# Kernel optimization log

Hardware: AMD Instinct MI355X
Metric: run time of the kernel (lower is better)

Reference implementation:

```python
import jax, jax.numpy as jnp
import numpy as np

N = 50000
E = 1600000
F_IN = 128
F_OUT = 64
NEG_SLOPE = 0.2


def setup_inputs() -> dict:
    key = jax.random.key(0)
    k1, k2, k3, k4, k5, k6 = jax.random.split(key, 6)
    x = jax.random.normal(k1, (N, F_IN), dtype=jnp.float32)
    edge_index = jax.random.randint(k2, (2, E), 0, N, dtype=jnp.int64)
    # GATConv params (heads=1): glorot-ish scale
    W = jax.random.normal(k3, (F_IN, F_OUT), dtype=jnp.float32) * (1.0 / np.sqrt(F_IN))
    att_src = jax.random.normal(k4, (F_OUT,), dtype=jnp.float32) * (1.0 / np.sqrt(F_OUT))
    att_dst = jax.random.normal(k5, (F_OUT,), dtype=jnp.float32) * (1.0 / np.sqrt(F_OUT))
    bias = jnp.zeros((F_OUT,), dtype=jnp.float32)
    return {"x": x, "edge_index": edge_index, "W": W, "att_src": att_src, "att_dst": att_dst, "bias": bias}


def _gat_forward(x, edge_index, W, att_src, att_dst, bias):
    n = x.shape[0]
    # add self loops (PyG GATConv default)
    loops = jnp.arange(n, dtype=edge_index.dtype)
    src = jnp.concatenate([edge_index[0], loops])  # [E+N]
    dst = jnp.concatenate([edge_index[1], loops])  # [E+N]

    h = x @ W                                      # [N, F_OUT]
    a_src = h @ att_src                            # [N]
    a_dst = h @ att_dst                            # [N]

    e = a_src[src] + a_dst[dst]                    # [E+N]
    e = jnp.where(e > 0, e, NEG_SLOPE * e)         # LeakyReLU(0.2)

    # softmax over edges grouped by destination node
    e_max = jax.ops.segment_max(e, dst, num_segments=n)     # [N]
    e_exp = jnp.exp(e - e_max[dst])                          # [E+N]
    e_sum = jax.ops.segment_sum(e_exp, dst, num_segments=n)  # [N]
    alpha = e_exp / e_sum[dst]                               # [E+N]

    msg = h[src] * alpha[:, None]                            # [E+N, F_OUT]
    out = jax.ops.segment_sum(msg, dst, num_segments=n)      # [N, F_OUT]
    out = out + bias
    return jax.nn.relu(out)


def reference(x, edge_index, W, att_src, att_dst, bias):
    return _gat_forward(x, edge_index, W, att_src, att_dst, bias)
```

## Files before the change

### kernel.cpp

```cpp
#include <hip/hip_runtime.h>

#define NN 50000
#define NE 1600000
#define FIN 128
#define FOUT 64
#define SLOPE 0.2f

#define NBC  63
#define NPC  800
#define CAPC 27500
#define NBF  1575
#define NPB  32
#define CAPB 1536
#define FBLK 261
#define CHC4 1536
#define GBLK 782
#define K2PB 8
#define LW   136

typedef unsigned int u32;
typedef short short8 __attribute__((ext_vector_type(8)));
typedef float f32x4 __attribute__((ext_vector_type(4)));

__device__ __forceinline__ unsigned short f2bf(float f) {
    u32 u = __float_as_uint(f);
    u += 0x7FFFu + ((u >> 16) & 1u);
    return (unsigned short)(u >> 16);
}
__device__ __forceinline__ float bf2f(unsigned short s) {
    return __uint_as_float(((u32)s) << 16);
}

union FusedLds {
    unsigned short Wt[64 * LW];
    struct { int cnt[4][64]; int gb[64]; int cur[64]; } f;
};

__global__ __launch_bounds__(256) void fused_k(
        const float* __restrict__ x, const float* __restrict__ W,
        const float* __restrict__ att_s, const float* __restrict__ att_d,
        const int* __restrict__ ei, int* __restrict__ ccur,
        u32* __restrict__ cstage, unsigned short* __restrict__ h,
        float* __restrict__ a_src, float* __restrict__ a_dst) {
    __shared__ FusedLds L;
    const int tid = threadIdx.x;

    if (blockIdx.x < FBLK) {
        const int wv = tid >> 6;
        ((int*)L.f.cnt)[tid] = 0;
        __syncthreads();
        const int4* sd4 = (const int4*)(ei + NE);
        const int4* ss4 = (const int4*)ei;
        const int lo = blockIdx.x * CHC4, hi = min(NE / 4, lo + CHC4);
        for (int i = lo + tid; i < hi; i += 256) {
            int4 d = sd4[i];
            atomicAdd(&L.f.cnt[wv][d.x / NPC], 1);
            atomicAdd(&L.f.cnt[wv][d.y / NPC], 1);
            atomicAdd(&L.f.cnt[wv][d.z / NPC], 1);
            atomicAdd(&L.f.cnt[wv][d.w / NPC], 1);
        }
        __syncthreads();
        if (tid < NBC) {
            int tot = L.f.cnt[0][tid] + L.f.cnt[1][tid]
                    + L.f.cnt[2][tid] + L.f.cnt[3][tid];
            L.f.gb[tid] = tot ? atomicAdd(&ccur[tid], tot) : 0;
            L.f.cur[tid] = 0;
        }
        __syncthreads();
        for (int i = lo + tid; i < hi; i += 256) {
            int4 d = sd4[i];
            int4 s = ss4[i];
            int b, pos;
            b = d.x / NPC; pos = L.f.gb[b] + atomicAdd(&L.f.cur[b], 1);
            if (pos < CAPC) cstage[b * CAPC + pos] = (u32)s.x | ((u32)(d.x - b * NPC) << 16);
            b = d.y / NPC; pos = L.f.gb[b] + atomicAdd(&L.f.cur[b], 1);
            if (pos < CAPC) cstage[b * CAPC + pos] = (u32)s.y | ((u32)(d.y - b * NPC) << 16);
            b = d.z / NPC; pos = L.f.gb[b] + atomicAdd(&L.f.cur[b], 1);
            if (pos < CAPC) cstage[b * CAPC + pos] = (u32)s.z | ((u32)(d.z - b * NPC) << 16);
            b = d.w / NPC; pos = L.f.gb[b] + atomicAdd(&L.f.cur[b], 1);
            if (pos < CAPC) cstage[b * CAPC + pos] = (u32)s.w | ((u32)(d.w - b * NPC) << 16);
        }
    } else {
        unsigned short* Wt = L.Wt;
        const int node0 = (blockIdx.x - FBLK) * 64;
        for (int i = tid; i < 128 * 16; i += 256) {
            int k = i >> 4, f = (i & 15) * 4;
            float4 w4 = ((const float4*)W)[i];
            Wt[(f + 0) * LW + k] = f2bf(w4.x);
            Wt[(f + 1) * LW + k] = f2bf(w4.y);
            Wt[(f + 2) * LW + k] = f2bf(w4.z);
            Wt[(f + 3) * LW + k] = f2bf(w4.w);
        }
        const int wv = tid >> 6, lane = tid & 63;
        const int q = lane >> 4, mr = lane & 15;
        const int row = node0 + wv * 16 + mr;
        const bool valid = row < NN;
        const float4* x4 = (const float4*)x;

        short8 afr[4];
        #pragma unroll
        for (int ks = 0; ks < 4; ++ks) {
            float4 f0 = make_float4(0.f, 0.f, 0.f, 0.f), f1 = f0;
            if (valid) {
                f0 = x4[(size_t)row * 32 + ks * 8 + q * 2];
                f1 = x4[(size_t)row * 32 + ks * 8 + q * 2 + 1];
            }
            short8 a;
            a[0] = (short)f2bf(f0.x); a[1] = (short)f2bf(f0.y);
            a[2] = (short)f2bf(f0.z); a[3] = (short)f2bf(f0.w);
            a[4] = (short)f2bf(f1.x); a[5] = (short)f2bf(f1.y);
            a[6] = (short)f2bf(f1.z); a[7] = (short)f2bf(f1.w);
            afr[ks] = a;
        }
        __syncthreads();

        f32x4 acc[4] = {{0,0,0,0},{0,0,0,0},{0,0,0,0},{0,0,0,0}};
        #pragma unroll
        for (int ks = 0; ks < 4; ++ks) {
            #pragma unroll
            for (int nt = 0; nt < 4; ++nt) {
                short8 b = *(const short8*)(Wt + (nt * 16 + mr) * LW + ks * 32 + q * 8);
                acc[nt] = __builtin_amdgcn_mfma_f32_16x16x32_bf16(afr[ks], b, acc[nt], 0, 0, 0);
            }
        }
        float atts[4], attd[4];
        #pragma unroll
        for (int nt = 0; nt < 4; ++nt) {
            atts[nt] = att_s[nt * 16 + mr];
            attd[nt] = att_d[nt * 16 + mr];
        }
        #pragma unroll
        for (int r = 0; r < 4; ++r) {
            int node = node0 + wv * 16 + q * 4 + r;
            float ps = 0.f, pd = 0.f;
            #pragma unroll
            for (int nt = 0; nt < 4; ++nt) {
                float v = acc[nt][r];
                if (node < NN) h[(size_t)node * 64 + nt * 16 + mr] = f2bf(v);
                ps += v * atts[nt];
                pd += v * attd[nt];
            }
            #pragma unroll
            for (int off = 8; off > 0; off >>= 1) {
                ps += __shfl_xor(ps, off);
                pd += __shfl_xor(pd, off);
            }
            if (mr == 0 && node < NN) { a_src[node] = ps; a_dst[node] = pd; }
        }
    }
}

__global__ __launch_bounds__(256) void fine_k(
        const u32* __restrict__ cstage, const int* __restrict__ ccur,
        int* __restrict__ fcur, u32* __restrict__ fstage) {
    const int bin = blockIdx.x / K2PB, sub = blockIdx.x % K2PB;
    const int size = min(ccur[bin], CAPC);
    const int qs = (size + K2PB - 1) / K2PB;
    const int lo = sub * qs, hi = min(size, lo + qs);
    const u32* src = cstage + (size_t)bin * CAPC;
    const int tid = threadIdx.x, wv = tid >> 6;

    __shared__ int cnt[4][32];
    __shared__ int gb[32];
    __shared__ int cur[32];
    ((int*)cnt)[tid & 127] = 0;
    __syncthreads();
    for (int i = lo + tid; i < hi; i += 256)
        atomicAdd(&cnt[wv][(src[i] >> 16) >> 5], 1);
    __syncthreads();
    if (tid < 25) {
        int tot = cnt[0][tid] + cnt[1][tid] + cnt[2][tid] + cnt[3][tid];
        gb[tid] = tot ? atomicAdd(&fcur[bin * 25 + tid], tot) : 0;
        cur[tid] = 0;
    }
    __syncthreads();
    for (int i = lo + tid; i < hi; i += 256) {
        u32 w = src[i];
        int dl = w >> 16;
        int f = dl >> 5;
        int pos = gb[f] + atomicAdd(&cur[f], 1);
        if (pos < CAPB)
            fstage[(size_t)(bin * 25 + f) * CAPB + pos] =
                (w & 0xFFFFu) | ((u32)(dl & 31) << 16);
    }
}

__global__ __launch_bounds__(256) void agg_k(
        const u32* __restrict__ staging, const int* __restrict__ bcur,
        const float* __restrict__ a_src, const float* __restrict__ a_dst,
        const ushort4* __restrict__ h4, const float* __restrict__ bias,
        float* __restrict__ out) {
    const int bkt = blockIdx.x;
    const int node0 = bkt << 5;
    if (node0 >= NN) return;
    const int nNodes = min(NPB, NN - node0);
    const int bsize = min(bcur[bkt], CAPB);
    const u32* stg = staging + (size_t)bkt * CAPB;
    const int tid = threadIdx.x, wv = tid >> 6, lane = tid & 63;

    __shared__ u32 pk[CAPB];
    __shared__ unsigned short ssrc[CAPB];
    __shared__ int lcnt[NPB];
    __shared__ int lbase[NPB + 1];
    __shared__ int lcur[NPB];
    float* evals = (float*)pk;

    for (int j = tid; j < bsize; j += 256) pk[j] = stg[j];
    if (tid < NPB) lcnt[tid] = 0;
    __syncthreads();
    for (int j = tid; j < bsize; j += 256)
        atomicAdd(&lcnt[pk[j] >> 16], 1);
    __syncthreads();
    if (tid < 64) {
        int v = (tid < NPB) ? lcnt[tid] : 0;
        #pragma unroll
        for (int off = 1; off < NPB; off <<= 1) {
            int u = __shfl_up(v, off);
            if (tid >= off) v += u;
        }
        if (tid < NPB) lbase[tid + 1] = v;
        if (tid == 0) lbase[0] = 0;
    }
    if (tid >= 64 && tid < 64 + NPB) lcur[tid - 64] = 0;
    __syncthreads();
    for (int j = tid; j < bsize; j += 256) {
        u32 w = pk[j];
        int ld = w >> 16;
        int pos = lbase[ld] + atomicAdd(&lcur[ld], 1);
        ssrc[pos] = (unsigned short)(w & 0xFFFFu);
    }
    __syncthreads();

    const int q = lane >> 4, ql = lane & 15;
    const float4 b4 = ((const float4*)bias)[ql];
    #pragma unroll
    for (int rnd = 0; rnd < 2; ++rnd) {
        const int ln = rnd * 16 + wv * 4 + q;
        if (ln >= nNodes) continue;
        const int n = node0 + ln;
        const int st = lbase[ln], deg = lbase[ln + 1] - st;
        const float ad = a_dst[n];
        float es = a_src[n] + ad; es = es > 0.f ? es : SLOPE * es;
        const float ps = __expf(es);
        float sum = 0.f;
        for (int j = ql; j < deg; j += 16) {
            int s = ssrc[st + j];
            float e = a_src[s] + ad; e = e > 0.f ? e : SLOPE * e;
            float pe = __expf(e);
            evals[st + j] = pe;
            sum += pe;
        }
        sum += __shfl_xor(sum, 8); sum += __shfl_xor(sum, 4);
        sum += __shfl_xor(sum, 2); sum += __shfl_xor(sum, 1);
        const float inv = 1.f / (sum + ps);

        ushort4 hs = h4[(size_t)n * 16 + ql];
        float a0 = ps * bf2f(hs.x), a1 = ps * bf2f(hs.y);
        float a2 = ps * bf2f(hs.z), a3 = ps * bf2f(hs.w);
        int j = 0;
        for (; j + 4 <= deg; j += 4) {
            int s0 = ssrc[st + j], s1 = ssrc[st + j + 1];
            int s2 = ssrc[st + j + 2], s3 = ssrc[st + j + 3];
            float e0 = evals[st + j], e1 = evals[st + j + 1];
            float e2 = evals[st + j + 2], e3 = evals[st + j + 3];
            ushort4 v0 = h4[(size_t)s0 * 16 + ql];
            ushort4 v1 = h4[(size_t)s1 * 16 + ql];
            ushort4 v2 = h4[(size_t)s2 * 16 + ql];
            ushort4 v3 = h4[(size_t)s3 * 16 + ql];
            a0 += e0 * bf2f(v0.x); a1 += e0 * bf2f(v0.y);
            a2 += e0 * bf2f(v0.z); a3 += e0 * bf2f(v0.w);
            a0 += e1 * bf2f(v1.x); a1 += e1 * bf2f(v1.y);
            a2 += e1 * bf2f(v1.z); a3 += e1 * bf2f(v1.w);
            a0 += e2 * bf2f(v2.x); a1 += e2 * bf2f(v2.y);
            a2 += e2 * bf2f(v2.z); a3 += e2 * bf2f(v2.w);
            a0 += e3 * bf2f(v3.x); a1 += e3 * bf2f(v3.y);
            a2 += e3 * bf2f(v3.z); a3 += e3 * bf2f(v3.w);
        }
        for (; j < deg; ++j) {
            int s = ssrc[st + j];
            float ev = evals[st + j];
            ushort4 hv = h4[(size_t)s * 16 + ql];
            a0 += ev * bf2f(hv.x); a1 += ev * bf2f(hv.y);
            a2 += ev * bf2f(hv.z); a3 += ev * bf2f(hv.w);
        }
        float4 o;
        o.x = a0 * inv + b4.x; o.x = o.x > 0.f ? o.x : 0.f;
        o.y = a1 * inv + b4.y; o.y = o.y > 0.f ? o.y : 0.f;
        o.z = a2 * inv + b4.z; o.z = o.z > 0.f ? o.z : 0.f;
        o.w = a3 * inv + b4.w; o.w = o.w > 0.f ? o.w : 0.f;
        ((float4*)out)[(size_t)n * 16 + ql] = o;
    }
}

extern "C" void kernel_launch(void* const* d_in, const int* in_sizes, int n_in,
                              void* d_out, int out_size, void* d_ws, size_t ws_size,
                              hipStream_t stream) {
    const float* x     = (const float*)d_in[0];
    const int*   ei    = (const int*)d_in[1];
    const float* W     = (const float*)d_in[2];
    const float* att_s = (const float*)d_in[3];
    const float* att_d = (const float*)d_in[4];
    const float* bias  = (const float*)d_in[5];
    float* out = (float*)d_out;

    unsigned short* h = (unsigned short*)d_ws;
    float* a_src  = (float*)(h + (size_t)NN * 64);
    float* a_dst  = a_src + NN;
    int*   ccur   = (int*)(a_dst + NN);
    int*   fcur   = ccur + 64;
    u32*   cstage = (u32*)(fcur + 1600);
    u32*   fstage = cstage + (size_t)NBC * CAPC;

    hipMemsetAsync(ccur, 0, (64 + 1600) * sizeof(int), stream);

    fused_k<<<FBLK + GBLK, 256, 0, stream>>>(x, W, att_s, att_d, ei, ccur,
                                             cstage, h, a_src, a_dst);
    fine_k<<<NBC * K2PB, 256, 0, stream>>>(cstage, ccur, fcur, fstage);
    agg_k<<<NBF, 256, 0, stream>>>(fstage, fcur, a_src, a_dst,
                                   (const ushort4*)h, bias, out);
}
```

Measured before the change: 145.2 us.

## Move GEMM from coarse-bin kernel into fine-bin kernel and halve coarse chunk size

The node-feature GEMM (h and attention scores) no longer runs alongside the coarse edge binning. It now runs in the same launch as the fine binning pass, and coarse binning gets its own kernel with twice as many blocks, each handling half the edges. The aim is to balance work across launches so the GEMM blocks overlap with the fine-bin blocks, and to give the coarse pass more parallelism. The cost is more global atomics on the coarse counters and a different kernel boundary placement.

```diff
diff --git a/kernel.cpp b/kernel.cpp
--- a/kernel.cpp
+++ b/kernel.cpp
@@ -12,10 +12,11 @@
 #define NBF  1575
 #define NPB  32
 #define CAPB 1536
-#define FBLK 261
-#define CHC4 1536
+#define FBLK 522
+#define CHC4 768
+#define K2PB 8
+#define FINB (NBC * K2PB)
 #define GBLK 782
-#define K2PB 8
 #define LW   136
 
 typedef unsigned int u32;
@@ -31,58 +32,93 @@
     return __uint_as_float(((u32)s) << 16);
 }
 
-union FusedLds {
+__global__ __launch_bounds__(256) void fill_k(
+        const int* __restrict__ ei, int* __restrict__ ccur,
+        u32* __restrict__ cstage) {
+    __shared__ int cnt[4][64];
+    __shared__ int gb[64];
+    __shared__ int cur[64];
+    const int tid = threadIdx.x, wv = tid >> 6;
+    ((int*)cnt)[tid] = 0;
+    __syncthreads();
+    const int4* sd4 = (const int4*)(ei + NE);
+    const int4* ss4 = (const int4*)ei;
+    const int lo = blockIdx.x * CHC4, hi = min(NE / 4, lo + CHC4);
+    for (int i = lo + tid; i < hi; i += 256) {
+        int4 d = sd4[i];
+        atomicAdd(&cnt[wv][d.x / NPC], 1);
+        atomicAdd(&cnt[wv][d.y / NPC], 1);
+        atomicAdd(&cnt[wv][d.z / NPC], 1);
+        atomicAdd(&cnt[wv][d.w / NPC], 1);
+    }
+    __syncthreads();
+    if (tid < NBC) {
+        int tot = cnt[0][tid] + cnt[1][tid] + cnt[2][tid] + cnt[3][tid];
+        gb[tid] = tot ? atomicAdd(&ccur[tid], tot) : 0;
+        cur[tid] = 0;
+    }
+    __syncthreads();
+    for (int i = lo + tid; i < hi; i += 256) {
+        int4 d = sd4[i];
+        int4 s = ss4[i];
+        int b, pos;
+        b = d.x / NPC; pos = gb[b] + atomicAdd(&cur[b], 1);
+        if (pos < CAPC) cstage[b * CAPC + pos] = (u32)s.x | ((u32)(d.x - b * NPC) << 16);
+        b = d.y / NPC; pos = gb[b] + atomicAdd(&cur[b], 1);
+        if (pos < CAPC) cstage[b * CAPC + pos] = (u32)s.y | ((u32)(d.y - b * NPC) << 16);
+        b = d.z / NPC; pos = gb[b] + atomicAdd(&cur[b], 1);
+        if (pos < CAPC) cstage[b * CAPC + pos] = (u32)s.z | ((u32)(d.z - b * NPC) << 16);
+        b = d.w / NPC; pos = gb[b] + atomicAdd(&cur[b], 1);
+        if (pos < CAPC) cstage[b * CAPC + pos] = (u32)s.w | ((u32)(d.w - b * NPC) << 16);
+    }
+}
+
+union FgLds {
     unsigned short Wt[64 * LW];
-    struct { int cnt[4][64]; int gb[64]; int cur[64]; } f;
+    struct { int cnt[4][32]; int gb[32]; int cur[32]; } f;
 };
 
-__global__ __launch_bounds__(256) void fused_k(
+__global__ __launch_bounds__(256) void fg_k(
+        const u32* __restrict__ cstage, const int* __restrict__ ccur,
+        int* __restrict__ fcur, u32* __restrict__ fstage,
         const float* __restrict__ x, const float* __restrict__ W,
         const float* __restrict__ att_s, const float* __restrict__ att_d,
-        const int* __restrict__ ei, int* __restrict__ ccur,
-        u32* __restrict__ cstage, unsigned short* __restrict__ h,
-        float* __restrict__ a_src, float* __restrict__ a_dst) {
-    __shared__ FusedLds L;
+        unsigned short* __restrict__ h, float* __restrict__ a_src,
+        float* __restrict__ a_dst) {
+    __shared__ FgLds L;
     const int tid = threadIdx.x;
 
-    if (blockIdx.x < FBLK) {
+    if (blockIdx.x < FINB) {
+        const int bin = blockIdx.x / K2PB, sub = blockIdx.x % K2PB;
+        const int size = min(ccur[bin], CAPC);
+        const int qs = (size + K2PB - 1) / K2PB;
+        const int lo = sub * qs, hi = min(size, lo + qs);
+        const u32* src = cstage + (size_t)bin * CAPC;
         const int wv = tid >> 6;
-        ((int*)L.f.cnt)[tid] = 0;
+        ((int*)L.f.cnt)[tid & 127] = 0;
         __syncthreads();
-        const int4* sd4 = (const int4*)(ei + NE);
-        const int4* ss4 = (const int4*)ei;
-        const int lo = blockIdx.x * CHC4, hi = min(NE / 4, lo + CHC4);
-        for (int i = lo + tid; i < hi; i += 256) {
-            int4 d = sd4[i];
-            atomicAdd(&L.f.cnt[wv][d.x / NPC], 1);
-            atomicAdd(&L.f.cnt[wv][d.y / NPC], 1);
-            atomicAdd(&L.f.cnt[wv][d.z / NPC], 1);
-            atomicAdd(&L.f.cnt[wv][d.w / NPC], 1);
-        }
+        for (int i = lo + tid; i < hi; i += 256)
+            atomicAdd(&L.f.cnt[wv][(src[i] >> 16) >> 5], 1);
         __syncthreads();
-        if (tid < NBC) {
+        if (tid < 25) {
             int tot = L.f.cnt[0][tid] + L.f.cnt[1][tid]
                     + L.f.cnt[2][tid] + L.f.cnt[3][tid];
-            L.f.gb[tid] = tot ? atomicAdd(&ccur[tid], tot) : 0;
+            L.f.gb[tid] = tot ? atomicAdd(&fcur[bin * 25 + tid], tot) : 0;
             L.f.cur[tid] = 0;
         }
         __syncthreads();
         for (int i = lo + tid; i < hi; i += 256) {
-            int4 d = sd4[i];
-            int4 s = ss4[i];
-            int b, pos;
-            b = d.x / NPC; pos = L.f.gb[b] + atomicAdd(&L.f.cur[b], 1);
-            if (pos < CAPC) cstage[b * CAPC + pos] = (u32)s.x | ((u32)(d.x - b * NPC) << 16);
-            b = d.y / NPC; pos = L.f.gb[b] + atomicAdd(&L.f.cur[b], 1);
-            if (pos < CAPC) cstage[b * CAPC + pos] = (u32)s.y | ((u32)(d.y - b * NPC) << 16);
-            b = d.z / NPC; pos = L.f.gb[b] + atomicAdd(&L.f.cur[b], 1);
-            if (pos < CAPC) cstage[b * CAPC + pos] = (u32)s.z | ((u32)(d.z - b * NPC) << 16);
-            b = d.w / NPC; pos = L.f.gb[b] + atomicAdd(&L.f.cur[b], 1);
-            if (pos < CAPC) cstage[b * CAPC + pos] = (u32)s.w | ((u32)(d.w - b * NPC) << 16);
+            u32 w = src[i];
+            int dl = w >> 16;
+            int f = dl >> 5;
+            int pos = L.f.gb[f] + atomicAdd(&L.f.cur[f], 1);
+            if (pos < CAPB)
+                fstage[(size_t)(bin * 25 + f) * CAPB + pos] =
+                    (w & 0xFFFFu) | ((u32)(dl & 31) << 16);
         }
     } else {
         unsigned short* Wt = L.Wt;
-        const int node0 = (blockIdx.x - FBLK) * 64;
+        const int node0 = (blockIdx.x - FINB) * 64;
         for (int i = tid; i < 128 * 16; i += 256) {
             int k = i >> 4, f = (i & 15) * 4;
             float4 w4 = ((const float4*)W)[i];
@@ -147,41 +183,6 @@
             }
             if (mr == 0 && node < NN) { a_src[node] = ps; a_dst[node] = pd; }
         }
-    }
-}
-
-__global__ __launch_bounds__(256) void fine_k(
-        const u32* __restrict__ cstage, const int* __restrict__ ccur,
-        int* __restrict__ fcur, u32* __restrict__ fstage) {
-    const int bin = blockIdx.x / K2PB, sub = blockIdx.x % K2PB;
-    const int size = min(ccur[bin], CAPC);
-    const int qs = (size + K2PB - 1) / K2PB;
-    const int lo = sub * qs, hi = min(size, lo + qs);
-    const u32* src = cstage + (size_t)bin * CAPC;
-    const int tid = threadIdx.x, wv = tid >> 6;
-
-    __shared__ int cnt[4][32];
-    __shared__ int gb[32];
-    __shared__ int cur[32];
-    ((int*)cnt)[tid & 127] = 0;
-    __syncthreads();
-    for (int i = lo + tid; i < hi; i += 256)
-        atomicAdd(&cnt[wv][(src[i] >> 16) >> 5], 1);
-    __syncthreads();
-    if (tid < 25) {
-        int tot = cnt[0][tid] + cnt[1][tid] + cnt[2][tid] + cnt[3][tid];
-        gb[tid] = tot ? atomicAdd(&fcur[bin * 25 + tid], tot) : 0;
-        cur[tid] = 0;
-    }
-    __syncthreads();
-    for (int i = lo + tid; i < hi; i += 256) {
-        u32 w = src[i];
-        int dl = w >> 16;
-        int f = dl >> 5;
-        int pos = gb[f] + atomicAdd(&cur[f], 1);
-        if (pos < CAPB)
-            fstage[(size_t)(bin * 25 + f) * CAPB + pos] =
-                (w & 0xFFFFu) | ((u32)(dl & 31) << 16);
     }
 }
 
@@ -313,9 +314,9 @@
 
     hipMemsetAsync(ccur, 0, (64 + 1600) * sizeof(int), stream);
 
-    fused_k<<<FBLK + GBLK, 256, 0, stream>>>(x, W, att_s, att_d, ei, ccur,
-                                             cstage, h, a_src, a_dst);
-    fine_k<<<NBC * K2PB, 256, 0, stream>>>(cstage, ccur, fcur, fstage);
+    fill_k<<<FBLK, 256, 0, stream>>>(ei, ccur, cstage);
+    fg_k<<<FINB + GBLK, 256, 0, stream>>>(cstage, ccur, fcur, fstage,
+                                          x, W, att_s, att_d, h, a_src, a_dst);
     agg_k<<<NBF, 256, 0, stream>>>(fstage, fcur, a_src, a_dst,
                                    (const ushort4*)h, bias, out);
 }
```

Result: no change. 146.1 us (+0.7%).
